# Kernel tuning notes

Measured on AMD Instinct MI355X. Metric: run time of the kernel, lower is better.

The kernel has to match this reference:

```python
import jax, jax.numpy as jnp
import numpy as np

B, N, DIM = 64, 1024, 64          # trees, type positions per tree, embedding dim
NUM_NODES = B * N                  # 65536 flattened type representations
E = 1_048_576                      # scope-goal edges
H = 4 * DIM                        # SwiGLU hidden width (=256)


def setup_inputs() -> dict:
    key = jax.random.key(0)
    k1, k2, k3, k4, k5 = jax.random.split(key, 5)
    type_reprs = jax.random.normal(k1, (B, N, DIM), dtype=jnp.float32)
    # SwiGLU(2*dim, 4*dim, 1): gate / value projections and output head (bias-free)
    w_gate = jax.random.normal(k2, (2 * DIM, H), dtype=jnp.float32) * (1.0 / np.sqrt(2 * DIM))
    w_in = jax.random.normal(k3, (2 * DIM, H), dtype=jnp.float32) * (1.0 / np.sqrt(2 * DIM))
    w_out = jax.random.normal(k4, (H, 1), dtype=jnp.float32) * (1.0 / np.sqrt(H))
    edge_index = jax.random.randint(k5, (2, E), 0, NUM_NODES, dtype=jnp.int64)
    return {
        "type_reprs": type_reprs,
        "w_gate": w_gate,
        "w_in": w_in,
        "w_out": w_out,
        "edge_index": edge_index,
    }


def reference(type_reprs, w_gate, w_in, w_out, edge_index):
    # flatten(0, 1): [B, N, dim] -> [B*N, dim]
    x = type_reprs.reshape(-1, type_reprs.shape[-1])
    scope_ids, goal_ids = edge_index[0], edge_index[1]
    # gather + concat: [E, 2*dim]
    features = jnp.concatenate((x[scope_ids], x[goal_ids]), axis=-1)
    # SwiGLU: silu(x @ Wg) * (x @ Wi) @ Wo
    hidden = jax.nn.silu(features @ w_gate) * (features @ w_in)  # [E, 4*dim]
    return (hidden @ w_out)[..., 0]                              # [E]
```

## Files before the change

### kernel.cpp

```cpp
#include <hip/hip_runtime.h>
#include <hip/hip_bf16.h>
#include <stdint.h>

#define NE      1048576
#define NNODES  65536
#define DIMV    64
#define HDIM    256

typedef __bf16 bf16x8 __attribute__((ext_vector_type(8)));
typedef float  f32x4  __attribute__((ext_vector_type(4)));
typedef float  f32x2  __attribute__((ext_vector_type(2)));

__device__ __forceinline__ unsigned short f2bf(float f) {
    union { float f; uint32_t u; } v; v.f = f;
    return (unsigned short)((v.u + 0x7fffu + ((v.u >> 16) & 1u)) >> 16);
}

__global__ void prep_x_kernel(const float* __restrict__ x, unsigned short* __restrict__ xb) {
    int i = blockIdx.x * blockDim.x + threadIdx.x;
    const int total = NNODES * DIMV / 4;
    for (; i < total; i += gridDim.x * blockDim.x) {
        float4 v = ((const float4*)x)[i];
        ushort4 o;
        o.x = f2bf(v.x); o.y = f2bf(v.y); o.z = f2bf(v.z); o.w = f2bf(v.w);
        ((ushort4*)xb)[i] = o;
    }
}

__global__ void prep_w_kernel(const float* __restrict__ wg, const float* __restrict__ wi,
                              const float* __restrict__ wo, unsigned short* __restrict__ img) {
    int t = blockIdx.x * blockDim.x + threadIdx.x;
    if (t >= 2 * HDIM * 16) return;
    int mat = t >> 12;
    int h   = (t >> 4) & 255;
    int cc  = t & 15;
    const float* w = mat ? wi : wg;
    float scale = mat ? wo[h] : 1.0f;
    unsigned short tmp[8] __attribute__((aligned(16)));
    #pragma unroll
    for (int j = 0; j < 8; ++j)
        tmp[j] = f2bf(w[(cc * 8 + j) * HDIM + h] * scale);
    int byteoff = mat * 65536 + h * 256 + ((cc * 16) ^ ((h & 7) << 4));
    *(uint4*)((char*)img + byteoff) = *(const uint4*)tmp;
}

#define EDGES_PER_BLOCK 128
__global__ __launch_bounds__(512)
void edge_swiglu_kernel(
    const unsigned short* __restrict__ xb,
    const unsigned short* __restrict__ wimg,
    const int* __restrict__ eidx,
    float* __restrict__ out)
{
    __shared__ char  alds[EDGES_PER_BLOCK * 256];
    __shared__ float plds[8][EDGES_PER_BLOCK];

    const int tid  = threadIdx.x;
    const int lane = tid & 63;
    const int wave = tid >> 6;
    const int r = lane & 15;
    const int q = lane >> 4;
    const int eb = blockIdx.x * EDGES_PER_BLOCK;

    #pragma unroll
    for (int i = 0; i < EDGES_PER_BLOCK * 16 / 512; ++i) {
        int idx  = i * 512 + tid;
        int el   = idx >> 4;
        int c    = idx & 15;
        int half = c >> 3;
        int srcc = (c & 7) ^ (el & 7);
        int e    = eb + el;
        int node = half ? eidx[NE + e] : eidx[e];
        const unsigned short* src = xb + node * 64 + srcc * 8;
        __builtin_amdgcn_global_load_lds(
            (const __attribute__((address_space(1))) void*)src,
            (__attribute__((address_space(3))) void*)(alds + idx * 16),
            16, 0, 0);
    }

    bf16x8 bw[2][2][4];
    #pragma unroll
    for (int nh = 0; nh < 2; ++nh) {
        int h      = (wave * 2 + nh) * 16 + r;
        int rowoff = h << 8;
        int swz    = (h & 7) << 4;
        #pragma unroll
        for (int mat = 0; mat < 2; ++mat) {
            #pragma unroll
            for (int ks = 0; ks < 4; ++ks) {
                int cb = ((4 * ks + q) * 16) ^ swz;
                bw[nh][mat][ks] = *(const bf16x8*)((const char*)wimg + mat * 65536 + rowoff + cb);
            }
        }
    }

    __syncthreads();

    #pragma unroll
    for (int mf = 0; mf < EDGES_PER_BLOCK / 16; ++mf) {
        const int   el   = mf * 16 + r;
        const char* arow = alds + el * 256;

        bf16x8 x[4];
        #pragma unroll
        for (int ks = 0; ks < 4; ++ks) {
            int ck = 4 * ks + q;
            int c  = (ck & 8) | ((ck & 7) ^ (r & 7));
            x[ks] = *(const bf16x8*)(arow + c * 16);
        }

        f32x2 part2 = {0.0f, 0.0f};
        #pragma unroll
        for (int nh = 0; nh < 2; ++nh) {
            f32x4 aG = {0.0f, 0.0f, 0.0f, 0.0f};
            f32x4 aI = {0.0f, 0.0f, 0.0f, 0.0f};
            #pragma unroll
            for (int ks = 0; ks < 4; ++ks) {
                aG = __builtin_amdgcn_mfma_f32_16x16x32_bf16(bw[nh][0][ks], x[ks], aG, 0, 0, 0);
                aI = __builtin_amdgcn_mfma_f32_16x16x32_bf16(bw[nh][1][ks], x[ks], aI, 0, 0, 0);
            }
            #pragma unroll
            for (int jj = 0; jj < 2; ++jj) {
                f32x2 g  = {aG[2 * jj], aG[2 * jj + 1]};
                f32x2 iv = {aI[2 * jj], aI[2 * jj + 1]};
                f32x2 t  = g * (f32x2){-1.44269504f, -1.44269504f};
                f32x2 ex = {__builtin_amdgcn_exp2f(t[0]), __builtin_amdgcn_exp2f(t[1])};
                f32x2 d  = ex + (f32x2){1.0f, 1.0f};
                f32x2 rc = {__builtin_amdgcn_rcpf(d[0]), __builtin_amdgcn_rcpf(d[1])};
                f32x2 u  = g * iv;
                part2 += u * rc;
            }
        }
        float part = part2[0] + part2[1];
        part += __shfl_xor(part, 16);
        part += __shfl_xor(part, 32);
        if (lane < 16) plds[wave][mf * 16 + lane] = part;
    }

    __syncthreads();

    if (tid < EDGES_PER_BLOCK) {
        float s = 0.0f;
        #pragma unroll
        for (int w = 0; w < 8; ++w) s += plds[w][tid];
        out[eb + tid] = s;
    }
}

extern "C" void kernel_launch(void* const* d_in, const int* in_sizes, int n_in,
                              void* d_out, int out_size, void* d_ws, size_t ws_size,
                              hipStream_t stream) {
    const float* x   = (const float*)d_in[0];
    const float* wg  = (const float*)d_in[1];
    const float* wi  = (const float*)d_in[2];
    const float* wo  = (const float*)d_in[3];
    const int*   ei  = (const int*)d_in[4];
    float* out = (float*)d_out;

    unsigned short* xb   = (unsigned short*)d_ws;
    unsigned short* wimg = (unsigned short*)((char*)d_ws + 8388608);

    prep_x_kernel<<<1024, 256, 0, stream>>>(x, xb);
    prep_w_kernel<<<32, 256, 0, stream>>>(wg, wi, wo, wimg);
    edge_swiglu_kernel<<<NE / EDGES_PER_BLOCK, 512, 0, stream>>>(xb, wimg, ei, out);
}
```

Baseline: 150.8 us.

## Double-buffer LDS gathers across four edge tiles per block

Each block now processes four 128-edge tiles instead of one. All edge indices are loaded up front, the weight fragments are loaded once per block, and the gather for tile t+1 is issued into a second LDS buffer while tile t is being computed. The aim is to hide gather latency behind MFMA work and to amortize weight-register loads over more edges. In exchange, LDS use per block roughly doubles and the grid is a quarter of its former size, which may lower occupancy.

```diff
diff --git a/kernel.cpp b/kernel.cpp
--- a/kernel.cpp
+++ b/kernel.cpp
@@ -44,7 +44,9 @@
     *(uint4*)((char*)img + byteoff) = *(const uint4*)tmp;
 }
 
-#define EDGES_PER_BLOCK 128
+#define EDGES_PER_TILE 128
+#define TILES 4
+#define EDGES_PER_BLOCK (EDGES_PER_TILE * TILES)
 __global__ __launch_bounds__(512)
 void edge_swiglu_kernel(
     const unsigned short* __restrict__ xb,
@@ -52,8 +54,8 @@
     const int* __restrict__ eidx,
     float* __restrict__ out)
 {
-    __shared__ char  alds[EDGES_PER_BLOCK * 256];
-    __shared__ float plds[8][EDGES_PER_BLOCK];
+    __shared__ char  alds[2][EDGES_PER_TILE * 256];
+    __shared__ float plds[8][EDGES_PER_TILE];
 
     const int tid  = threadIdx.x;
     const int lane = tid & 63;
@@ -62,20 +64,17 @@
     const int q = lane >> 4;
     const int eb = blockIdx.x * EDGES_PER_BLOCK;
 
+    int nodes[TILES][4];
     #pragma unroll
-    for (int i = 0; i < EDGES_PER_BLOCK * 16 / 512; ++i) {
-        int idx  = i * 512 + tid;
-        int el   = idx >> 4;
-        int c    = idx & 15;
-        int half = c >> 3;
-        int srcc = (c & 7) ^ (el & 7);
-        int e    = eb + el;
-        int node = half ? eidx[NE + e] : eidx[e];
-        const unsigned short* src = xb + node * 64 + srcc * 8;
-        __builtin_amdgcn_global_load_lds(
-            (const __attribute__((address_space(1))) void*)src,
-            (__attribute__((address_space(3))) void*)(alds + idx * 16),
-            16, 0, 0);
+    for (int t = 0; t < TILES; ++t) {
+        #pragma unroll
+        for (int i = 0; i < 4; ++i) {
+            int idx = i * 512 + tid;
+            int el  = idx >> 4;
+            int c   = idx & 15;
+            int e   = eb + t * EDGES_PER_TILE + el;
+            nodes[t][i] = (c & 8) ? eidx[NE + e] : eidx[e];
+        }
     }
 
     bf16x8 bw[2][2][4];
@@ -94,56 +93,88 @@
         }
     }
 
-    __syncthreads();
+    #pragma unroll
+    for (int i = 0; i < 4; ++i) {
+        int idx  = i * 512 + tid;
+        int el   = idx >> 4;
+        int c    = idx & 15;
+        int srcc = (c & 7) ^ (el & 7);
+        const unsigned short* src = xb + nodes[0][i] * 64 + srcc * 8;
+        __builtin_amdgcn_global_load_lds(
+            (const __attribute__((address_space(1))) void*)src,
+            (__attribute__((address_space(3))) void*)(alds[0] + idx * 16),
+            16, 0, 0);
+    }
 
     #pragma unroll
-    for (int mf = 0; mf < EDGES_PER_BLOCK / 16; ++mf) {
-        const int   el   = mf * 16 + r;
-        const char* arow = alds + el * 256;
+    for (int t = 0; t < TILES; ++t) {
+        __syncthreads();
 
-        bf16x8 x[4];
-        #pragma unroll
-        for (int ks = 0; ks < 4; ++ks) {
-            int ck = 4 * ks + q;
-            int c  = (ck & 8) | ((ck & 7) ^ (r & 7));
-            x[ks] = *(const bf16x8*)(arow + c * 16);
+        if (t + 1 < TILES) {
+            #pragma unroll
+            for (int i = 0; i < 4; ++i) {
+                int idx  = i * 512 + tid;
+                int el   = idx >> 4;
+                int c    = idx & 15;
+                int srcc = (c & 7) ^ (el & 7);
+                const unsigned short* src = xb + nodes[t + 1][i] * 64 + srcc * 8;
+                __builtin_amdgcn_global_load_lds(
+                    (const __attribute__((address_space(1))) void*)src,
+                    (__attribute__((address_space(3))) void*)(alds[(t + 1) & 1] + idx * 16),
+                    16, 0, 0);
+            }
         }
 
-        f32x2 part2 = {0.0f, 0.0f};
+        const char* abuf = alds[t & 1];
         #pragma unroll
-        for (int nh = 0; nh < 2; ++nh) {
-            f32x4 aG = {0.0f, 0.0f, 0.0f, 0.0f};
-            f32x4 aI = {0.0f, 0.0f, 0.0f, 0.0f};
+        for (int mf = 0; mf < EDGES_PER_TILE / 16; ++mf) {
+            const int   el   = mf * 16 + r;
+            const char* arow = abuf + el * 256;
+
+            bf16x8 x[4];
             #pragma unroll
             for (int ks = 0; ks < 4; ++ks) {
-                aG = __builtin_amdgcn_mfma_f32_16x16x32_bf16(bw[nh][0][ks], x[ks], aG, 0, 0, 0);
-                aI = __builtin_amdgcn_mfma_f32_16x16x32_bf16(bw[nh][1][ks], x[ks], aI, 0, 0, 0);
+                int ck = 4 * ks + q;
+                int c  = (ck & 8) | ((ck & 7) ^ (r & 7));
+                x[ks] = *(const bf16x8*)(arow + c * 16);
             }
+
+            f32x2 part2 = {0.0f, 0.0f};
             #pragma unroll
-            for (int jj = 0; jj < 2; ++jj) {
-                f32x2 g  = {aG[2 * jj], aG[2 * jj + 1]};
-                f32x2 iv = {aI[2 * jj], aI[2 * jj + 1]};
-                f32x2 t  = g * (f32x2){-1.44269504f, -1.44269504f};
-                f32x2 ex = {__builtin_amdgcn_exp2f(t[0]), __builtin_amdgcn_exp2f(t[1])};
-                f32x2 d  = ex + (f32x2){1.0f, 1.0f};
-                f32x2 rc = {__builtin_amdgcn_rcpf(d[0]), __builtin_amdgcn_rcpf(d[1])};
-                f32x2 u  = g * iv;
-                part2 += u * rc;
+            for (int nh = 0; nh < 2; ++nh) {
+                f32x4 aG = {0.0f, 0.0f, 0.0f, 0.0f};
+                f32x4 aI = {0.0f, 0.0f, 0.0f, 0.0f};
+                #pragma unroll
+                for (int ks = 0; ks < 4; ++ks) {
+                    aG = __builtin_amdgcn_mfma_f32_16x16x32_bf16(bw[nh][0][ks], x[ks], aG, 0, 0, 0);
+                    aI = __builtin_amdgcn_mfma_f32_16x16x32_bf16(bw[nh][1][ks], x[ks], aI, 0, 0, 0);
+                }
+                #pragma unroll
+                for (int jj = 0; jj < 2; ++jj) {
+                    f32x2 g  = {aG[2 * jj], aG[2 * jj + 1]};
+                    f32x2 iv = {aI[2 * jj], aI[2 * jj + 1]};
+                    f32x2 tt = g * (f32x2){-1.44269504f, -1.44269504f};
+                    f32x2 ex = {__builtin_amdgcn_exp2f(tt[0]), __builtin_amdgcn_exp2f(tt[1])};
+                    f32x2 d  = ex + (f32x2){1.0f, 1.0f};
+                    f32x2 rc = {__builtin_amdgcn_rcpf(d[0]), __builtin_amdgcn_rcpf(d[1])};
+                    f32x2 u  = g * iv;
+                    part2 += u * rc;
+                }
             }
+            float part = part2[0] + part2[1];
+            part += __shfl_xor(part, 16);
+            part += __shfl_xor(part, 32);
+            if (lane < 16) plds[wave][mf * 16 + lane] = part;
         }
-        float part = part2[0] + part2[1];
-        part += __shfl_xor(part, 16);
-        part += __shfl_xor(part, 32);
-        if (lane < 16) plds[wave][mf * 16 + lane] = part;
-    }
 
-    __syncthreads();
+        __syncthreads();
 
-    if (tid < EDGES_PER_BLOCK) {
-        float s = 0.0f;
-        #pragma unroll
-        for (int w = 0; w < 8; ++w) s += plds[w][tid];
-        out[eb + tid] = s;
+        if (tid < EDGES_PER_TILE) {
+            float s = 0.0f;
+            #pragma unroll
+            for (int w = 0; w < 8; ++w) s += plds[w][tid];
+            out[eb + t * EDGES_PER_TILE + tid] = s;
+        }
     }
 }
 
```

Measured after the change: 144.8 us. -4.0%, faster.
